# Kernel optimization log

Measured on AMD Instinct MI355X. Metric: run time of the kernel, lower is better.

The kernel has to match this reference:

```python
import jax, jax.numpy as jnp
import numpy as np

DIM = 512
HEADS = 8
P = 4  # split_size
SCALE = (DIM // HEADS) ** -0.5  # scale uses full dim//heads as in source


def conv1x1(x, w):
    # x: [b,c,h,w], w: [out,in]
    return jnp.einsum('oc,bchw->bohw', w, x)


def to_windows(t, p1, p2, h):
    # 'b (h d) (x p1) (y p2) -> (b x y) h (p1 p2) d'
    b, c, X, Y = t.shape
    d = c // h
    nx, ny = X // p1, Y // p2
    t = t.reshape(b, h, d, nx, p1, ny, p2)
    t = t.transpose(0, 3, 5, 1, 4, 6, 2)  # b nx ny h p1 p2 d
    return t.reshape(b * nx * ny, h, p1 * p2, d)


def from_windows(t, b, nx, ny, h, p1, p2, d):
    # '(b x y) h (p1 p2) d -> b (h d) (x p1) (y p2)'
    t = t.reshape(b, nx, ny, h, p1, p2, d)
    t = t.transpose(0, 3, 6, 1, 4, 2, 5)  # b h d nx p1 ny p2
    return t.reshape(b, h * d, nx * p1, ny * p2)


def setup_inputs() -> dict:
    key = jax.random.key(0)
    ks = jax.random.split(key, 6)
    s = 0.02
    return {
        'fmap': jax.random.normal(ks[0], (8, DIM, 64, 64), jnp.float32),
        'w_qk': jax.random.normal(ks[1], (2 * DIM, DIM), jnp.float32) * s,
        'w_v': jax.random.normal(ks[2], (DIM, DIM), jnp.float32) * s,
        'w_v_vert': jax.random.normal(ks[3], (DIM // 2, DIM // 2), jnp.float32) * s,
        'w_v_horiz': jax.random.normal(ks[4], (DIM // 2, DIM // 2), jnp.float32) * s,
        'w_proj': jax.random.normal(ks[5], (DIM, DIM), jnp.float32) * s,
    }


def reference(fmap, w_qk, w_v, w_v_vert, w_v_horiz, w_proj):
    b, c, X, Y = fmap.shape
    h, half = HEADS, c // 2
    d = half // h  # per-window head dim

    qk = conv1x1(fmap, w_qk)
    q, k = jnp.split(qk, 2, axis=1)
    v = conv1x1(fmap, w_v)

    # horizontal branch: first half channels, windows (X, P)
    qh = to_windows(q[:, :half], X, P, h)
    kh = to_windows(k[:, :half], X, P, h)
    vh = to_windows(v[:, :half], X, P, h)
    lepe_h = vh  # source bug: to_v_horizontal output discarded, raw v used as LePE

    # vertical branch: second half channels, windows (P, Y)
    qv = to_windows(q[:, half:], P, Y, h)
    kv = to_windows(k[:, half:], P, Y, h)
    vv = to_windows(v[:, half:], P, Y, h)
    lepe_v = to_windows(conv1x1(v[:, half:], w_v_vert), P, Y, h)

    def attend(qw, kw, vw, lepe):
        attn = jax.nn.softmax((qw * SCALE) @ jnp.swapaxes(kw, -1, -2), axis=-1)
        return attn @ vw + lepe

    out_h = attend(qh, kh, vh, lepe_h)
    out_v = attend(qv, kv, vv, lepe_v)

    oh = from_windows(out_h, b, X // X, Y // P, h, X, P, d)
    ov = from_windows(out_v, b, X // P, Y // Y, h, P, Y, d)
    out = jnp.concatenate([oh, ov], axis=1)
    return fmap + conv1x1(out, w_proj)
```

## Files before the change

### kernel.cpp

```cpp
#include <hip/hip_runtime.h>
#include <hip/hip_bf16.h>

#define NPIX 4096
#define SCALE_L2E 0.18033688f

typedef unsigned short ushort_t;
typedef __attribute__((ext_vector_type(8))) short bf16x8;
typedef __attribute__((ext_vector_type(4))) float f32x4;
typedef __attribute__((ext_vector_type(8))) unsigned short us8;

__device__ __forceinline__ float bf2f(ushort_t u) {
  union { unsigned int i; float f; } v; v.i = ((unsigned int)u) << 16; return v.f;
}
__device__ __forceinline__ ushort_t f2bf(float f) {
  union { float f; unsigned int i; } v; v.f = f;
  unsigned int r = v.i + 0x7fffu + ((v.i >> 16) & 1u);
  return (ushort_t)(r >> 16);
}
__device__ __forceinline__ unsigned int cvtpk(float lo, float hi) {
  unsigned int r;
  asm volatile("v_cvt_pk_bf16_f32 %0, %1, %2" : "=v"(r) : "v"(lo), "v"(hi));
  return r;
}

__device__ __forceinline__ void gload16(const void* g, void* l) {
  __builtin_amdgcn_global_load_lds(
      (const __attribute__((address_space(1))) void*)g,
      (__attribute__((address_space(3))) void*)l, 16, 0, 0);
}

__global__ __launch_bounds__(256) void cast_bf16(const float* __restrict__ s,
                                                 ushort_t* __restrict__ d, int n,
                                                 float scale) {
  int i = (blockIdx.x * 256 + threadIdx.x) * 4;
  if (i < n) {
    float4 v = *(const float4*)&s[i];
    ushort4 o = make_ushort4(f2bf(v.x * scale), f2bf(v.y * scale),
                             f2bf(v.z * scale), f2bf(v.w * scale));
    *(ushort4*)&d[i] = o;
  }
}

__global__ __launch_bounds__(256) void lepe_w(const float* __restrict__ wvv,
                                              const float* __restrict__ wv,
                                              ushort_t* __restrict__ out) {
  const int i = blockIdx.x, tid = threadIdx.x;
  float a0 = 0.f, a1 = 0.f;
  for (int c = 0; c < 256; ++c) {
    const float wc = wvv[i * 256 + c];
    a0 = fmaf(wc, wv[(size_t)(256 + c) * 512 + tid], a0);
    a1 = fmaf(wc, wv[(size_t)(256 + c) * 512 + 256 + tid], a1);
  }
  out[(size_t)i * 512 + tid] = f2bf(a0);
  out[(size_t)i * 512 + 256 + tid] = f2bf(a1);
}

__global__ __launch_bounds__(256) void transpose_cast(const float* __restrict__ fmap,
                                                      ushort_t* __restrict__ XT) {
  const int b = blockIdx.z, p0 = blockIdx.x * 64, c0 = blockIdx.y * 64;
  const int tid = threadIdx.x;
  __shared__ float t[64][65];
  const float* src = fmap + ((size_t)b * 512 + c0) * NPIX + p0;
  const int pr = tid & 63;
  #pragma unroll
  for (int i = 0; i < 16; ++i) {
    const int cr = i * 4 + (tid >> 6);
    t[cr][pr] = src[(size_t)cr * NPIX + pr];
  }
  __syncthreads();
  const int pw = tid >> 2, cwb = (tid & 3) * 16;
  us8 o0, o1;
  #pragma unroll
  for (int i = 0; i < 8; ++i) o0[i] = f2bf(t[cwb + i][pw]);
  #pragma unroll
  for (int i = 0; i < 8; ++i) o1[i] = f2bf(t[cwb + 8 + i][pw]);
  ushort_t* dst = XT + ((size_t)b * NPIX + p0 + pw) * 512 + c0 + cwb;
  *(us8*)&dst[0] = o0;
  *(us8*)&dst[8] = o1;
}

__global__ __launch_bounds__(256) void gemm_mfma(
    const ushort_t* __restrict__ A, const ushort_t* __restrict__ B,
    void* __restrict__ Cout, void* __restrict__ Cout2,
    const float* __restrict__ Res,
    long bStrideB, long bStrideC, long bStrideC2, int mode)
{
  const int b = blockIdx.z;
  const int p0 = blockIdx.x * 128;
  const int o0 = blockIdx.y * 128;
  const int tid = threadIdx.x;
  const int lane = tid & 63, w = tid >> 6;
  const int wrow = (w >> 1) * 64, wcol = (w & 1) * 64;

  __shared__ __attribute__((aligned(16))) short As[128 * 32];
  __shared__ __attribute__((aligned(16))) short Bs[128 * 32];

  const ushort_t* Bb = B + (size_t)b * bStrideB;

  f32x4 acc[4][4];
  #pragma unroll
  for (int m = 0; m < 4; ++m)
    #pragma unroll
    for (int n = 0; n < 4; ++n) acc[m][n] = (f32x4){0.f, 0.f, 0.f, 0.f};

  const int cl = lane & 3;

  for (int kt = 0; kt < 16; ++kt) {
    const int kb = kt * 32;
    #pragma unroll
    for (int i = 0; i < 2; ++i) {
      const int r = w * 32 + i * 16 + (lane >> 2);
      const int cs = cl ^ ((r >> 1) & 3);
      gload16(&A[(size_t)(o0 + r) * 512 + kb + cs * 8], &As[(w * 32 + i * 16) * 32]);
      gload16(&Bb[(size_t)(p0 + r) * 512 + kb + cs * 8], &Bs[(w * 32 + i * 16) * 32]);
    }
    __syncthreads();
    bf16x8 af[4], bfr[4];
    #pragma unroll
    for (int m = 0; m < 4; ++m) {
      const int row = wrow + m * 16 + (lane & 15);
      const int c = (lane >> 4) ^ ((row >> 1) & 3);
      af[m] = *(const bf16x8*)&As[row * 32 + c * 8];
    }
    #pragma unroll
    for (int n = 0; n < 4; ++n) {
      const int row = wcol + n * 16 + (lane & 15);
      const int c = (lane >> 4) ^ ((row >> 1) & 3);
      bfr[n] = *(const bf16x8*)&Bs[row * 32 + c * 8];
    }
    #pragma unroll
    for (int m = 0; m < 4; ++m)
      #pragma unroll
      for (int n = 0; n < 4; ++n)
        acc[m][n] = __builtin_amdgcn_mfma_f32_16x16x32_bf16(af[m], bfr[n], acc[m][n], 0, 0, 0);
    __syncthreads();
  }

  const int fr = lane & 15, fq = lane >> 4;
  if (mode == 3) {
    if (o0 < 1024) {
      ushort_t* CT = (ushort_t*)Cout + (size_t)b * bStrideC;
      #pragma unroll
      for (int m = 0; m < 4; ++m)
        #pragma unroll
        for (int n = 0; n < 4; ++n) {
          const int pix = p0 + wcol + n * 16 + fr;
          const int chb = o0 + wrow + m * 16 + fq * 4;
          ushort4 s4 = make_ushort4(f2bf(acc[m][n][0]), f2bf(acc[m][n][1]),
                                    f2bf(acc[m][n][2]), f2bf(acc[m][n][3]));
          *(ushort4*)&CT[(size_t)pix * 1024 + chb] = s4;
        }
    } else {
      ushort_t* C = (ushort_t*)Cout2 + (size_t)b * bStrideC2;
      #pragma unroll
      for (int m = 0; m < 4; ++m)
        #pragma unroll
        for (int n = 0; n < 4; ++n) {
          const int col = p0 + wcol + n * 16 + fr;
          #pragma unroll
          for (int j = 0; j < 4; ++j) {
            const int row = o0 - 1024 + wrow + m * 16 + fq * 4 + j;
            C[(size_t)row * NPIX + col] = f2bf(acc[m][n][j]);
          }
        }
    }
  } else {
    float* C = (float*)Cout + (size_t)b * bStrideC;
    const float* R = Res + (size_t)b * bStrideC;
    #pragma unroll
    for (int m = 0; m < 4; ++m)
      #pragma unroll
      for (int n = 0; n < 4; ++n) {
        const int col = p0 + wcol + n * 16 + fr;
        #pragma unroll
        for (int j = 0; j < 4; ++j) {
          const int row = o0 + wrow + m * 16 + fq * 4 + j;
          const size_t idx = (size_t)row * NPIX + col;
          C[idx] = acc[m][n][j] + R[idx];
        }
      }
  }
}

__global__ __launch_bounds__(256) void attn_mfma(const ushort_t* __restrict__ qkT,
                                                 const ushort_t* __restrict__ vbuf,
                                                 ushort_t* __restrict__ attT) {
  const int hh = blockIdx.x, wi = blockIdx.y, vert = blockIdx.z;
  const int b = wi >> 4, iw = wi & 15;
  const int tid = threadIdx.x;
  const int lane = tid & 63, w = tid >> 6;
  const int g = lane >> 4, q16 = lane & 15;
  const int qbase = w * 64;

  __shared__ __attribute__((aligned(16))) ushort_t K_lds[256 * 32];
  __shared__ __attribute__((aligned(16))) ushort_t VT_lds[32 * 256];
  __shared__ __attribute__((aligned(16))) ushort_t P_lds[4][64 * 40];

  const ushort_t* QKb = qkT + (size_t)b * NPIX * 1024;

  #pragma unroll
  for (int it = 0; it < 4; ++it) {
    const int j = w * 64 + it * 16 + (lane >> 2);
    const int cs = (lane & 3) ^ ((j >> 1) & 3);
    const int pj = vert ? iw * 256 + j : (j >> 2) * 64 + iw * 4 + (j & 3);
    gload16(&QKb[(size_t)pj * 1024 + 512 + hh * 32 + cs * 8],
            &K_lds[(w * 64 + it * 16) * 32]);
  }
  const ushort_t* Vg = vbuf + ((size_t)b * 768 + vert * 256 + hh * 32) * (size_t)NPIX;
  #pragma unroll
  for (int it = 0; it < 8; ++it) {
    const int d = it * 4 + w;
    const int jg = lane;
    const int pb = vert ? iw * 256 + jg * 4 : jg * 64 + iw * 4;
    const ushort4 v4 = *(const ushort4*)&Vg[(size_t)d * NPIX + pb];
    *(ushort4*)&VT_lds[d * 256 + (((jg >> 1) ^ d) << 3) + ((jg & 1) << 2)] = v4;
  }
  bf16x8 qf[4];
  #pragma unroll
  for (int qt = 0; qt < 4; ++qt) {
    const int q = qbase + qt * 16 + q16;
    const int qp = vert ? iw * 256 + q : (q >> 2) * 64 + iw * 4 + (q & 3);
    qf[qt] = *(const bf16x8*)&QKb[(size_t)qp * 1024 + hh * 32 + g * 8];
  }
  __syncthreads();

  float l[4] = {0.f, 0.f, 0.f, 0.f};
  f32x4 o[4][2];
  #pragma unroll
  for (int qt = 0; qt < 4; ++qt) {
    o[qt][0] = (f32x4){0.f, 0.f, 0.f, 0.f};
    o[qt][1] = (f32x4){0.f, 0.f, 0.f, 0.f};
  }

  const f32x4 zero4 = (f32x4){0.f, 0.f, 0.f, 0.f};
  const int kc = g ^ ((q16 >> 1) & 3);

  for (int jc = 0; jc < 8; ++jc) {
    bf16x8 kf0 = *(const bf16x8*)&K_lds[(jc * 32 + q16) * 32 + kc * 8];
    bf16x8 kf1 = *(const bf16x8*)&K_lds[(jc * 32 + 16 + q16) * 32 + kc * 8];
    f32x4 st[2][4];
    #pragma unroll
    for (int qt = 0; qt < 4; ++qt) {
      st[0][qt] = __builtin_amdgcn_mfma_f32_16x16x32_bf16(kf0, qf[qt], zero4, 0, 0, 0);
      st[1][qt] = __builtin_amdgcn_mfma_f32_16x16x32_bf16(kf1, qf[qt], zero4, 0, 0, 0);
    }
    #pragma unroll
    for (int qt = 0; qt < 4; ++qt) {
      const float p00 = exp2f(st[0][qt][0]), p01 = exp2f(st[0][qt][1]);
      const float p02 = exp2f(st[0][qt][2]), p03 = exp2f(st[0][qt][3]);
      const float p10 = exp2f(st[1][qt][0]), p11 = exp2f(st[1][qt][1]);
      const float p12 = exp2f(st[1][qt][2]), p13 = exp2f(st[1][qt][3]);
      float rs = ((p00 + p01) + (p02 + p03)) + ((p10 + p11) + (p12 + p13));
      rs += __shfl_xor(rs, 16);
      rs += __shfl_xor(rs, 32);
      l[qt] += rs;
      uint2 pk0, pk1;
      pk0.x = cvtpk(p00, p01); pk0.y = cvtpk(p02, p03);
      pk1.x = cvtpk(p10, p11); pk1.y = cvtpk(p12, p13);
      *(uint2*)&P_lds[w][(qt * 16 + q16) * 40 + g * 4]      = pk0;
      *(uint2*)&P_lds[w][(qt * 16 + q16) * 40 + 16 + g * 4] = pk1;
    }
    const int vc0 = (jc * 4 + g) ^ q16;
    const int vc1 = (jc * 4 + g) ^ (16 + q16);
    bf16x8 vf0 = *(const bf16x8*)&VT_lds[q16 * 256 + vc0 * 8];
    bf16x8 vf1 = *(const bf16x8*)&VT_lds[(16 + q16) * 256 + vc1 * 8];
    #pragma unroll
    for (int qt = 0; qt < 4; ++qt) {
      bf16x8 pf = *(const bf16x8*)&P_lds[w][(qt * 16 + q16) * 40 + g * 8];
      o[qt][0] = __builtin_amdgcn_mfma_f32_16x16x32_bf16(pf, vf0, o[qt][0], 0, 0, 0);
      o[qt][1] = __builtin_amdgcn_mfma_f32_16x16x32_bf16(pf, vf1, o[qt][1], 0, 0, 0);
    }
  }

  const int ch = vert * 256 + hh * 32;
  const ushort_t* Lg = vbuf + ((size_t)b * 768 + 512 + hh * 32) * (size_t)NPIX;
  #pragma unroll
  for (int qt = 0; qt < 4; ++qt) {
    const float linv = 1.f / l[qt];
    float li[4];
    #pragma unroll
    for (int jj = 0; jj < 4; ++jj) li[jj] = __shfl(linv, g * 4 + jj);
    #pragma unroll
    for (int dt = 0; dt < 2; ++dt) {
      const int d = dt * 16 + q16;
      #pragma unroll
      for (int jj = 0; jj < 4; ++jj) {
        const int q = qbase + qt * 16 + g * 4 + jj;
        float lep;
        if (vert) lep = bf2f(Lg[(size_t)d * NPIX + iw * 256 + q]);
        else      lep = bf2f(VT_lds[d * 256 + (((q >> 3) ^ d) << 3) + (q & 7)]);
        const int pix = vert ? iw * 256 + q : (q >> 2) * 64 + iw * 4 + (q & 3);
        attT[((size_t)b * NPIX + pix) * 512 + ch + d] = f2bf(o[qt][dt][jj] * li[jj] + lep);
      }
    }
  }
}

extern "C" void kernel_launch(void* const* d_in, const int* in_sizes, int n_in,
                              void* d_out, int out_size, void* d_ws, size_t ws_size,
                              hipStream_t stream) {
  const float* fmap     = (const float*)d_in[0];
  const float* w_qk     = (const float*)d_in[1];
  const float* w_v      = (const float*)d_in[2];
  const float* w_v_vert = (const float*)d_in[3];
  const float* w_proj   = (const float*)d_in[5];
  float* out = (float*)d_out;

  ushort_t* XT   = (ushort_t*)d_ws;
  ushort_t* qkT  = XT + (size_t)8 * NPIX * 512;
  ushort_t* vbuf = qkT + (size_t)8 * NPIX * 1024;
  ushort_t* attT = vbuf + (size_t)8 * 768 * NPIX;
  ushort_t* WQKV = attT + (size_t)8 * NPIX * 512;
  ushort_t* WPb  = WQKV + (size_t)1792 * 512;

  dim3 blk(256);
  cast_bf16<<<256, blk, 0, stream>>>(w_qk, WQKV, 512 * 512, SCALE_L2E);
  cast_bf16<<<256, blk, 0, stream>>>(w_qk + (size_t)512 * 512,
                                     WQKV + (size_t)512 * 512, 512 * 512, 1.0f);
  cast_bf16<<<256, blk, 0, stream>>>(w_v, WQKV + (size_t)1024 * 512, 512 * 512, 1.0f);
  cast_bf16<<<256, blk, 0, stream>>>(w_proj, WPb, 512 * 512, 1.0f);
  lepe_w<<<256, blk, 0, stream>>>(w_v_vert, w_v, WQKV + (size_t)1536 * 512);
  transpose_cast<<<dim3(64, 8, 8), blk, 0, stream>>>(fmap, XT);
  gemm_mfma<<<dim3(32, 14, 8), blk, 0, stream>>>(
      WQKV, XT, qkT, vbuf, nullptr,
      (long)NPIX * 512, (long)NPIX * 1024, (long)768 * NPIX, 3);
  attn_mfma<<<dim3(8, 128, 2), blk, 0, stream>>>(qkT, vbuf, attT);
  gemm_mfma<<<dim3(32, 4, 8), blk, 0, stream>>>(
      WPb, attT, out, nullptr, fmap,
      (long)NPIX * 512, (long)512 * NPIX, 0, 1);
}
```

Baseline: 251.2 us.

## Replace QKV projection GEMM with 256x256-tile double-buffered pipelined kernel

The fused QK/V/LePE projection GEMM moves to a new 512-thread kernel with 256x256 output tiles and a 64-wide K step. It double-buffers LDS, issues global-to-LDS loads for the next stage between MFMA quarters, and uses explicit waitcnt, barrier and setprio scheduling. The goal is to hide load latency and raise data reuse per block. The cost is a grid of only 896 blocks at one block per CU and high register and LDS pressure. The projection GEMM is split into its own simplified kernel.

Result: faster. 237.0 us (-5.7%).

```diff
diff --git a/kernel.cpp b/kernel.cpp
--- a/kernel.cpp
+++ b/kernel.cpp
@@ -28,6 +28,12 @@
       (const __attribute__((address_space(1))) void*)g,
       (__attribute__((address_space(3))) void*)l, 16, 0, 0);
 }
+
+#define VMW(N) do { asm volatile("s_waitcnt vmcnt(" #N ")" ::: "memory"); \
+                    __builtin_amdgcn_sched_barrier(0); } while (0)
+#define LGKM0  do { asm volatile("s_waitcnt lgkmcnt(0)" ::: "memory");    \
+                    __builtin_amdgcn_sched_barrier(0); } while (0)
+#define BARR   __builtin_amdgcn_s_barrier()
 
 __global__ __launch_bounds__(256) void cast_bf16(const float* __restrict__ s,
                                                  ushort_t* __restrict__ d, int n,
@@ -79,11 +85,160 @@
   *(us8*)&dst[8] = o1;
 }
 
-__global__ __launch_bounds__(256) void gemm_mfma(
+__global__ __launch_bounds__(512, 1) void gemm256(
     const ushort_t* __restrict__ A, const ushort_t* __restrict__ B,
-    void* __restrict__ Cout, void* __restrict__ Cout2,
-    const float* __restrict__ Res,
-    long bStrideB, long bStrideC, long bStrideC2, int mode)
+    ushort_t* __restrict__ qkT, ushort_t* __restrict__ vbuf)
+{
+  const int b = blockIdx.z;
+  const int p0 = blockIdx.x * 256;
+  const int o0 = blockIdx.y * 256;
+  const int tid = threadIdx.x;
+  const int lane = tid & 63, w = tid >> 6;
+  const int wm = w >> 2, wn = w & 3;
+  const int g = lane >> 4, q16 = lane & 15;
+  const int rl = lane >> 3, cc = lane & 7;
+  const int cs = cc ^ rl;
+
+  __shared__ __attribute__((aligned(16))) ushort_t lds[2 * 32768];
+
+  const ushort_t* Bb = B + (size_t)b * NPIX * 512;
+
+  f32x4 acc[8][4];
+  #pragma unroll
+  for (int m = 0; m < 8; ++m)
+    #pragma unroll
+    for (int n = 0; n < 4; ++n) acc[m][n] = (f32x4){0.f, 0.f, 0.f, 0.f};
+
+  auto AHp = [&](int buf, int H) { return lds + buf * 32768 + H * 8192; };
+  auto BHp = [&](int buf, int H) { return lds + buf * 32768 + 16384 + H * 8192; };
+
+  auto stageA = [&](int buf, int H, int kb) {
+    #pragma unroll
+    for (int i = 0; i < 2; ++i) {
+      const int row_g = o0 + i * 128 + H * 64 + w * 8 + rl;
+      gload16(&A[(size_t)row_g * 512 + kb + cs * 8],
+              AHp(buf, H) + (i * 64 + w * 8) * 64);
+    }
+  };
+  auto stageB = [&](int buf, int H, int kb) {
+    #pragma unroll
+    for (int i = 0; i < 2; ++i) {
+      const int stripe = i * 2 + (w >> 2);
+      const int within = (w & 3) * 8 + rl;
+      const int row_g = p0 + stripe * 64 + H * 32 + within;
+      gload16(&Bb[(size_t)row_g * 512 + kb + cs * 8],
+              BHp(buf, H) + (stripe * 32 + (w & 3) * 8) * 64);
+    }
+  };
+  bf16x8 a[4][2], b01[2][2], b23[2][2];
+  auto loadA = [&](int buf, int H) {
+    #pragma unroll
+    for (int mf = 0; mf < 4; ++mf)
+      #pragma unroll
+      for (int kk = 0; kk < 2; ++kk) {
+        const int rr = wm * 64 + mf * 16 + q16;
+        a[mf][kk] = *(const bf16x8*)&AHp(buf, H)[rr * 64 + ((kk * 4 + g) ^ (q16 & 7)) * 8];
+      }
+  };
+  auto loadB = [&](bf16x8 bb[2][2], int buf, int H) {
+    #pragma unroll
+    for (int nf = 0; nf < 2; ++nf)
+      #pragma unroll
+      for (int kk = 0; kk < 2; ++kk) {
+        const int rr = wn * 32 + nf * 16 + q16;
+        bb[nf][kk] = *(const bf16x8*)&BHp(buf, H)[rr * 64 + ((kk * 4 + g) ^ (q16 & 7)) * 8];
+      }
+  };
+
+#define MMA_Q(MH, NH, BB)                                                      \
+  do {                                                                         \
+    __builtin_amdgcn_s_setprio(1);                                             \
+    _Pragma("unroll")                                                          \
+    for (int mf = 0; mf < 4; ++mf)                                             \
+      _Pragma("unroll")                                                        \
+      for (int nf = 0; nf < 2; ++nf)                                           \
+        _Pragma("unroll")                                                      \
+        for (int kk = 0; kk < 2; ++kk)                                         \
+          acc[(MH) * 4 + mf][(NH) * 2 + nf] =                                  \
+              __builtin_amdgcn_mfma_f32_16x16x32_bf16(                         \
+                  a[mf][kk], BB[nf][kk], acc[(MH) * 4 + mf][(NH) * 2 + nf],    \
+                  0, 0, 0);                                                    \
+    __builtin_amdgcn_s_setprio(0);                                             \
+  } while (0)
+
+  stageA(0, 0, 0); stageB(0, 0, 0); stageB(0, 1, 0); stageA(0, 1, 0);
+  VMW(4);
+  BARR;
+
+  #pragma unroll 1
+  for (int kt = 0; kt < 7; ++kt) {
+    const int c = kt & 1, n = c ^ 1;
+    const int kn = (kt + 1) * 64;
+    loadA(c, 0); loadB(b01, c, 0);
+    stageA(n, 0, kn);
+    LGKM0;
+    MMA_Q(0, 0, b01);
+    VMW(4); BARR;
+    loadB(b23, c, 1);
+    stageB(n, 0, kn);
+    LGKM0;
+    MMA_Q(0, 1, b23);
+    VMW(4); BARR;
+    loadA(c, 1);
+    stageB(n, 1, kn);
+    LGKM0;
+    MMA_Q(1, 1, b23);
+    stageA(n, 1, kn);
+    MMA_Q(1, 0, b01);
+    VMW(4); BARR;
+  }
+  {
+    loadA(1, 0); loadB(b01, 1, 0);
+    LGKM0;
+    MMA_Q(0, 0, b01);
+    VMW(2); BARR;
+    loadB(b23, 1, 1);
+    LGKM0;
+    MMA_Q(0, 1, b23);
+    VMW(0); BARR;
+    loadA(1, 1);
+    LGKM0;
+    MMA_Q(1, 1, b23);
+    MMA_Q(1, 0, b01);
+  }
+
+  if (o0 < 1024) {
+    ushort_t* CT = qkT + (size_t)b * NPIX * 1024;
+    #pragma unroll
+    for (int mf = 0; mf < 8; ++mf)
+      #pragma unroll
+      for (int nf = 0; nf < 4; ++nf) {
+        const int pix = p0 + wn * 64 + nf * 16 + q16;
+        const int chb = o0 + wm * 128 + mf * 16 + g * 4;
+        ushort4 s4 = make_ushort4(f2bf(acc[mf][nf][0]), f2bf(acc[mf][nf][1]),
+                                  f2bf(acc[mf][nf][2]), f2bf(acc[mf][nf][3]));
+        *(ushort4*)&CT[(size_t)pix * 1024 + chb] = s4;
+      }
+  } else {
+    ushort_t* C = vbuf + (size_t)b * 768 * NPIX;
+    #pragma unroll
+    for (int mf = 0; mf < 8; ++mf)
+      #pragma unroll
+      for (int nf = 0; nf < 4; ++nf) {
+        const int col = p0 + wn * 64 + nf * 16 + q16;
+        #pragma unroll
+        for (int j = 0; j < 4; ++j) {
+          const int row = o0 - 1024 + wm * 128 + mf * 16 + g * 4 + j;
+          C[(size_t)row * NPIX + col] = f2bf(acc[mf][nf][j]);
+        }
+      }
+  }
+#undef MMA_Q
+}
+
+__global__ __launch_bounds__(256) void gemm_proj(
+    const ushort_t* __restrict__ A, const ushort_t* __restrict__ B,
+    float* __restrict__ Cout, const float* __restrict__ Res)
 {
   const int b = blockIdx.z;
   const int p0 = blockIdx.x * 128;
@@ -95,7 +250,7 @@
   __shared__ __attribute__((aligned(16))) short As[128 * 32];
   __shared__ __attribute__((aligned(16))) short Bs[128 * 32];
 
-  const ushort_t* Bb = B + (size_t)b * bStrideB;
+  const ushort_t* Bb = B + (size_t)b * NPIX * 512;
 
   f32x4 acc[4][4];
   #pragma unroll
@@ -137,49 +292,20 @@
   }
 
   const int fr = lane & 15, fq = lane >> 4;
-  if (mode == 3) {
-    if (o0 < 1024) {
-      ushort_t* CT = (ushort_t*)Cout + (size_t)b * bStrideC;
-      #pragma unroll
-      for (int m = 0; m < 4; ++m)
-        #pragma unroll
-        for (int n = 0; n < 4; ++n) {
-          const int pix = p0 + wcol + n * 16 + fr;
-          const int chb = o0 + wrow + m * 16 + fq * 4;
-          ushort4 s4 = make_ushort4(f2bf(acc[m][n][0]), f2bf(acc[m][n][1]),
-                                    f2bf(acc[m][n][2]), f2bf(acc[m][n][3]));
-          *(ushort4*)&CT[(size_t)pix * 1024 + chb] = s4;
-        }
-    } else {
-      ushort_t* C = (ushort_t*)Cout2 + (size_t)b * bStrideC2;
-      #pragma unroll
-      for (int m = 0; m < 4; ++m)
-        #pragma unroll
-        for (int n = 0; n < 4; ++n) {
-          const int col = p0 + wcol + n * 16 + fr;
-          #pragma unroll
-          for (int j = 0; j < 4; ++j) {
-            const int row = o0 - 1024 + wrow + m * 16 + fq * 4 + j;
-            C[(size_t)row * NPIX + col] = f2bf(acc[m][n][j]);
-          }
-        }
-    }
-  } else {
-    float* C = (float*)Cout + (size_t)b * bStrideC;
-    const float* R = Res + (size_t)b * bStrideC;
-    #pragma unroll
-    for (int m = 0; m < 4; ++m)
-      #pragma unroll
-      for (int n = 0; n < 4; ++n) {
-        const int col = p0 + wcol + n * 16 + fr;
-        #pragma unroll
-        for (int j = 0; j < 4; ++j) {
-          const int row = o0 + wrow + m * 16 + fq * 4 + j;
-          const size_t idx = (size_t)row * NPIX + col;
-          C[idx] = acc[m][n][j] + R[idx];
-        }
-      }
-  }
+  float* C = Cout + (size_t)b * 512 * NPIX;
+  const float* R = Res + (size_t)b * 512 * NPIX;
+  #pragma unroll
+  for (int m = 0; m < 4; ++m)
+    #pragma unroll
+    for (int n = 0; n < 4; ++n) {
+      const int col = p0 + wcol + n * 16 + fr;
+      #pragma unroll
+      for (int j = 0; j < 4; ++j) {
+        const int row = o0 + wrow + m * 16 + fq * 4 + j;
+        const size_t idx = (size_t)row * NPIX + col;
+        C[idx] = acc[m][n][j] + R[idx];
+      }
+    }
 }
 
 __global__ __launch_bounds__(256) void attn_mfma(const ushort_t* __restrict__ qkT,
@@ -321,11 +447,7 @@
   cast_bf16<<<256, blk, 0, stream>>>(w_proj, WPb, 512 * 512, 1.0f);
   lepe_w<<<256, blk, 0, stream>>>(w_v_vert, w_v, WQKV + (size_t)1536 * 512);
   transpose_cast<<<dim3(64, 8, 8), blk, 0, stream>>>(fmap, XT);
-  gemm_mfma<<<dim3(32, 14, 8), blk, 0, stream>>>(
-      WQKV, XT, qkT, vbuf, nullptr,
-      (long)NPIX * 512, (long)NPIX * 1024, (long)768 * NPIX, 3);
+  gemm256<<<dim3(16, 7, 8), dim3(512), 0, stream>>>(WQKV, XT, qkT, vbuf);
   attn_mfma<<<dim3(8, 128, 2), blk, 0, stream>>>(qkT, vbuf, attT);
-  gemm_mfma<<<dim3(32, 4, 8), blk, 0, stream>>>(
-      WPb, attT, out, nullptr, fmap,
-      (long)NPIX * 512, (long)512 * NPIX, 0, 1);
-}
+  gemm_proj<<<dim3(32, 4, 8), blk, 0, stream>>>(WPb, attT, out, fmap);
+}
```

## Triple-buffer GEMM LDS staging and merge weight cast kernels

Applied to the files above, without the earlier changes.

The GEMM now uses a three-stage LDS ring, prefetching two K-tiles ahead with explicit vmcnt waits and a single barrier per iteration instead of two __syncthreads. It also raises wave priority around the MFMA block and folds the four weight-cast launches into one kernel. The aim is to hide global-load latency behind MFMA work and cut launch overhead, at the cost of three times the LDS footprint, which may reduce occupancy.

Measured after the change: 224.1 us. 1.12x faster.

```diff
diff --git a/kernel.cpp b/kernel.cpp
--- a/kernel.cpp
+++ b/kernel.cpp
@@ -29,16 +29,30 @@
       (__attribute__((address_space(3))) void*)l, 16, 0, 0);
 }
 
-__global__ __launch_bounds__(256) void cast_bf16(const float* __restrict__ s,
-                                                 ushort_t* __restrict__ d, int n,
-                                                 float scale) {
-  int i = (blockIdx.x * 256 + threadIdx.x) * 4;
-  if (i < n) {
-    float4 v = *(const float4*)&s[i];
-    ushort4 o = make_ushort4(f2bf(v.x * scale), f2bf(v.y * scale),
-                             f2bf(v.z * scale), f2bf(v.w * scale));
-    *(ushort4*)&d[i] = o;
-  }
+#define VMW(N) do { asm volatile("s_waitcnt vmcnt(" #N ")" ::: "memory"); \
+                    __builtin_amdgcn_sched_barrier(0); } while (0)
+#define LGKM0  do { asm volatile("s_waitcnt lgkmcnt(0)" ::: "memory");    \
+                    __builtin_amdgcn_sched_barrier(0); } while (0)
+#define BARR   __builtin_amdgcn_s_barrier()
+
+__global__ __launch_bounds__(256) void prep_w(const float* __restrict__ wqk,
+                                              const float* __restrict__ wv,
+                                              const float* __restrict__ wproj,
+                                              ushort_t* __restrict__ WQKV,
+                                              ushort_t* __restrict__ WPb) {
+  const int i = (blockIdx.x * 256 + threadIdx.x) * 4;
+  const int seg = i >> 18, off = i & 262143;
+  const float* src;
+  ushort_t* dst;
+  float sc = 1.0f;
+  if (seg == 0)      { src = wqk;          dst = WQKV;               sc = SCALE_L2E; }
+  else if (seg == 1) { src = wqk + 262144; dst = WQKV + 262144; }
+  else if (seg == 2) { src = wv;           dst = WQKV + 2 * 262144; }
+  else               { src = wproj;        dst = WPb; }
+  const float4 v = *(const float4*)&src[off];
+  ushort4 o = make_ushort4(f2bf(v.x * sc), f2bf(v.y * sc),
+                           f2bf(v.z * sc), f2bf(v.w * sc));
+  *(ushort4*)&dst[off] = o;
 }
 
 __global__ __launch_bounds__(256) void lepe_w(const float* __restrict__ wvv,
@@ -79,11 +93,10 @@
   *(us8*)&dst[8] = o1;
 }
 
-__global__ __launch_bounds__(256) void gemm_mfma(
+__global__ __launch_bounds__(256) void gemm128(
     const ushort_t* __restrict__ A, const ushort_t* __restrict__ B,
-    void* __restrict__ Cout, void* __restrict__ Cout2,
-    const float* __restrict__ Res,
-    long bStrideB, long bStrideC, long bStrideC2, int mode)
+    ushort_t* __restrict__ qkT, ushort_t* __restrict__ vbuf,
+    float* __restrict__ outF, const float* __restrict__ Res, int mode)
 {
   const int b = blockIdx.z;
   const int p0 = blockIdx.x * 128;
@@ -91,11 +104,11 @@
   const int tid = threadIdx.x;
   const int lane = tid & 63, w = tid >> 6;
   const int wrow = (w >> 1) * 64, wcol = (w & 1) * 64;
-
-  __shared__ __attribute__((aligned(16))) short As[128 * 32];
-  __shared__ __attribute__((aligned(16))) short Bs[128 * 32];
-
-  const ushort_t* Bb = B + (size_t)b * bStrideB;
+  const int g = lane >> 4, q16 = lane & 15;
+
+  __shared__ __attribute__((aligned(16))) ushort_t lds[3 * 8192];
+
+  const ushort_t* Bb = B + (size_t)b * NPIX * 512;
 
   f32x4 acc[4][4];
   #pragma unroll
@@ -103,43 +116,55 @@
     #pragma unroll
     for (int n = 0; n < 4; ++n) acc[m][n] = (f32x4){0.f, 0.f, 0.f, 0.f};
 
-  const int cl = lane & 3;
-
-  for (int kt = 0; kt < 16; ++kt) {
-    const int kb = kt * 32;
+  auto Ap = [&](int buf) { return lds + buf * 8192; };
+  auto Bp = [&](int buf) { return lds + buf * 8192 + 4096; };
+
+  auto stage = [&](int buf, int kb) {
     #pragma unroll
     for (int i = 0; i < 2; ++i) {
       const int r = w * 32 + i * 16 + (lane >> 2);
-      const int cs = cl ^ ((r >> 1) & 3);
-      gload16(&A[(size_t)(o0 + r) * 512 + kb + cs * 8], &As[(w * 32 + i * 16) * 32]);
-      gload16(&Bb[(size_t)(p0 + r) * 512 + kb + cs * 8], &Bs[(w * 32 + i * 16) * 32]);
-    }
-    __syncthreads();
+      const int cs = (lane & 3) ^ ((r >> 1) & 3);
+      gload16(&A[(size_t)(o0 + r) * 512 + kb + cs * 8], Ap(buf) + (w * 32 + i * 16) * 32);
+      gload16(&Bb[(size_t)(p0 + r) * 512 + kb + cs * 8], Bp(buf) + (w * 32 + i * 16) * 32);
+    }
+  };
+
+  stage(0, 0);
+  stage(1, 32);
+  VMW(4);
+  BARR;
+
+  #pragma unroll
+  for (int kt = 0; kt < 16; ++kt) {
+    const int c = kt % 3;
+    if (kt < 14) stage((kt + 2) % 3, (kt + 2) * 32);
     bf16x8 af[4], bfr[4];
     #pragma unroll
     for (int m = 0; m < 4; ++m) {
-      const int row = wrow + m * 16 + (lane & 15);
-      const int c = (lane >> 4) ^ ((row >> 1) & 3);
-      af[m] = *(const bf16x8*)&As[row * 32 + c * 8];
+      const int rr = wrow + m * 16 + q16;
+      af[m] = *(const bf16x8*)&Ap(c)[rr * 32 + (g ^ ((rr >> 1) & 3)) * 8];
     }
     #pragma unroll
     for (int n = 0; n < 4; ++n) {
-      const int row = wcol + n * 16 + (lane & 15);
-      const int c = (lane >> 4) ^ ((row >> 1) & 3);
-      bfr[n] = *(const bf16x8*)&Bs[row * 32 + c * 8];
-    }
+      const int rr = wcol + n * 16 + q16;
+      bfr[n] = *(const bf16x8*)&Bp(c)[rr * 32 + (g ^ ((rr >> 1) & 3)) * 8];
+    }
+    LGKM0;
+    __builtin_amdgcn_s_setprio(1);
     #pragma unroll
     for (int m = 0; m < 4; ++m)
       #pragma unroll
       for (int n = 0; n < 4; ++n)
         acc[m][n] = __builtin_amdgcn_mfma_f32_16x16x32_bf16(af[m], bfr[n], acc[m][n], 0, 0, 0);
-    __syncthreads();
+    __builtin_amdgcn_s_setprio(0);
+    if (kt < 14) { VMW(4); BARR; }
+    else if (kt == 14) { VMW(0); BARR; }
   }
 
   const int fr = lane & 15, fq = lane >> 4;
-  if (mode == 3) {
+  if (mode == 0) {
     if (o0 < 1024) {
-      ushort_t* CT = (ushort_t*)Cout + (size_t)b * bStrideC;
+      ushort_t* CT = qkT + (size_t)b * NPIX * 1024;
       #pragma unroll
       for (int m = 0; m < 4; ++m)
         #pragma unroll
@@ -151,7 +176,7 @@
           *(ushort4*)&CT[(size_t)pix * 1024 + chb] = s4;
         }
     } else {
-      ushort_t* C = (ushort_t*)Cout2 + (size_t)b * bStrideC2;
+      ushort_t* C = vbuf + (size_t)b * 768 * NPIX;
       #pragma unroll
       for (int m = 0; m < 4; ++m)
         #pragma unroll
@@ -165,8 +190,8 @@
         }
     }
   } else {
-    float* C = (float*)Cout + (size_t)b * bStrideC;
-    const float* R = Res + (size_t)b * bStrideC;
+    float* C = outF + (size_t)b * 512 * NPIX;
+    const float* R = Res + (size_t)b * 512 * NPIX;
     #pragma unroll
     for (int m = 0; m < 4; ++m)
       #pragma unroll
@@ -314,18 +339,12 @@
   ushort_t* WPb  = WQKV + (size_t)1792 * 512;
 
   dim3 blk(256);
-  cast_bf16<<<256, blk, 0, stream>>>(w_qk, WQKV, 512 * 512, SCALE_L2E);
-  cast_bf16<<<256, blk, 0, stream>>>(w_qk + (size_t)512 * 512,
-                                     WQKV + (size_t)512 * 512, 512 * 512, 1.0f);
-  cast_bf16<<<256, blk, 0, stream>>>(w_v, WQKV + (size_t)1024 * 512, 512 * 512, 1.0f);
-  cast_bf16<<<256, blk, 0, stream>>>(w_proj, WPb, 512 * 512, 1.0f);
+  prep_w<<<1024, blk, 0, stream>>>(w_qk, w_v, w_proj, WQKV, WPb);
   lepe_w<<<256, blk, 0, stream>>>(w_v_vert, w_v, WQKV + (size_t)1536 * 512);
   transpose_cast<<<dim3(64, 8, 8), blk, 0, stream>>>(fmap, XT);
-  gemm_mfma<<<dim3(32, 14, 8), blk, 0, stream>>>(
-      WQKV, XT, qkT, vbuf, nullptr,
-      (long)NPIX * 512, (long)NPIX * 1024, (long)768 * NPIX, 3);
+  gemm128<<<dim3(32, 14, 8), blk, 0, stream>>>(
+      WQKV, XT, qkT, vbuf, nullptr, nullptr, 0);
   attn_mfma<<<dim3(8, 128, 2), blk, 0, stream>>>(qkT, vbuf, attT);
-  gemm_mfma<<<dim3(32, 4, 8), blk, 0, stream>>>(
-      WPb, attT, out, nullptr, fmap,
-      (long)NPIX * 512, (long)512 * NPIX, 0, 1);
-}
+  gemm128<<<dim3(32, 4, 8), blk, 0, stream>>>(
+      WPb, attT, nullptr, nullptr, out, fmap, 1);
+}
```
